# Performance work log

Measured on AMD Instinct MI355X. Metric: run time of the kernel, lower is better.

Reference implementation:

```python
import jax, jax.numpy as jnp
import numpy as np

B, N, H = 32, 2048, 128


def _lstm_step(c, h, x, Wi, Wh, b):
    # flax LSTMCell: gates i,f,g,o; sigmoid/sigmoid/tanh/sigmoid
    gates = x @ Wi + h @ Wh + b  # (B,N,4H)
    i, f, g, o = jnp.split(gates, 4, axis=-1)
    c_new = jax.nn.sigmoid(f) * c + jax.nn.sigmoid(i) * jnp.tanh(g)
    h_new = jax.nn.sigmoid(o) * jnp.tanh(c_new)
    return c_new, h_new


def setup_inputs() -> dict:
    key = jax.random.key(0)
    ks = jax.random.split(key, 24)
    f32 = jnp.float32
    inp = {}
    inp['node_embeddings'] = jax.random.normal(ks[0], (B, N, H), f32)
    for nm, k in zip(['hs_c0', 'hs_h0', 'hs_c1', 'hs_h1'], ks[1:5]):
        inp[nm] = jax.random.normal(k, (B, N, H), f32)
    ip = jax.random.uniform(ks[5], (B, N), f32)
    inp['instruction_pointer'] = ip / jnp.sum(ip, axis=-1, keepdims=True)
    inp['Wi0'] = jax.random.normal(ks[6], (H, 4 * H), f32) * 0.05
    inp['Wh0'] = jax.random.normal(ks[7], (H, 4 * H), f32) * 0.05
    inp['b0'] = jnp.zeros((4 * H,), f32)
    inp['Wi1'] = jax.random.normal(ks[8], (H, 4 * H), f32) * 0.05
    inp['Wh1'] = jax.random.normal(ks[9], (H, 4 * H), f32) * 0.05
    inp['b1'] = jnp.zeros((4 * H,), f32)
    inp['W_raise'] = jax.random.normal(ks[10], (4 * H, 2), f32) * 0.05
    inp['b_raise'] = jnp.zeros((2,), f32)
    inp['W_branch'] = jax.random.normal(ks[11], (4 * H, 2), f32) * 0.05
    inp['b_branch'] = jnp.zeros((2,), f32)
    inp['true_indexes'] = jax.random.randint(ks[12], (B, N), 0, N, jnp.int32)
    inp['false_indexes'] = jax.random.randint(ks[13], (B, N), 0, N, jnp.int32)
    inp['raise_indexes'] = jax.random.randint(ks[14], (B, N), 0, N, jnp.int32)
    inp['exit_node_indexes'] = jax.random.randint(ks[15], (B,), 0, N, jnp.int32)
    inp['raise_node_indexes'] = jax.random.randint(ks[16], (B,), 0, N, jnp.int32)
    inp['step_limits'] = jax.random.randint(ks[17], (B,), 0, 100, jnp.int32)
    inp['current_step'] = 5
    return inp


def reference(node_embeddings, hs_c0, hs_h0, hs_c1, hs_h1, instruction_pointer,
              Wi0, Wh0, b0, Wi1, Wh1, b1, W_raise, b_raise, W_branch, b_branch,
              true_indexes, false_indexes, raise_indexes,
              exit_node_indexes, raise_node_indexes, step_limits, current_step):
    bidx = jnp.arange(B)
    old = [hs_c0, hs_h0, hs_c1, hs_h1]

    # execute: per-node 2-layer stacked LSTM (vectorized over B,N)
    c0n, h0n = _lstm_step(hs_c0, hs_h0, node_embeddings, Wi0, Wh0, b0)
    c1n, h1n = _lstm_step(hs_c1, hs_h1, h0n, Wi1, Wh1, b1)
    contrib = [c0n, h0n, c1n, h1n]

    # mask_h: keep old state at exit node and (raise_in_ipagnn) at raise node
    def mask_nodes(hc, ho, idx):
        return hc.at[bidx, idx].set(ho[bidx, idx])
    contrib = [mask_nodes(mask_nodes(hc, ho, exit_node_indexes), ho, raise_node_indexes)
               for hc, ho in zip(contrib, old)]

    hs_emb = jnp.concatenate(contrib, axis=-1)  # (B,N,4H)

    raise_dec = jax.nn.softmax(hs_emb @ W_raise + b_raise, axis=-1)
    zero_one = jnp.array([0.0, 1.0], dtype=raise_dec.dtype)
    raise_dec = raise_dec.at[bidx, exit_node_indexes].set(zero_one)
    raise_dec = raise_dec.at[bidx, raise_node_indexes].set(zero_one)
    branch_dec = jax.nn.softmax(hs_emb @ W_branch + b_branch, axis=-1)

    p_raise = raise_dec[..., 0]
    p_noraise = raise_dec[..., 1]
    p_true = p_noraise * branch_dec[..., 0]
    p_false = p_noraise * branch_dec[..., 1]

    seg = jax.vmap(lambda v, idx: jax.ops.segment_sum(v, idx, num_segments=N))
    ip = instruction_pointer
    ip_new = (seg(p_raise * ip, raise_indexes)
              + seg(p_true * ip, true_indexes)
              + seg(p_false * ip, false_indexes))  # (B,N)
    denom = (ip_new + 1e-7)[..., None]

    wr = (p_raise * ip)[..., None]
    wt = (p_true * ip)[..., None]
    wf = (p_false * ip)[..., None]

    def agg(h):
        return (seg(h * wr, raise_indexes) + seg(h * wt, true_indexes)
                + seg(h * wf, false_indexes)) / denom
    hs_new = [agg(h) for h in contrib]

    # keep_old_if_done
    not_done = (current_step < step_limits)  # (B,)
    hs_out = [jnp.where(not_done[:, None, None], hn, ho) for hn, ho in zip(hs_new, old)]
    ip_out = jnp.where(not_done[:, None], ip_new, ip)

    # pack carry: (c0,h0,c1,h1, instruction_pointer) -> (B,N,4H+1)
    return jnp.concatenate(hs_out + [ip_out[..., None]], axis=-1)
```

## Files before the change

kernel.cpp:

```cpp
#include <hip/hip_runtime.h>
#include <stdint.h>

#define BB 32
#define NN 2048
#define HH 128
#define BN (BB*NN)

typedef short v8s __attribute__((ext_vector_type(8)));
typedef float v4f __attribute__((ext_vector_type(4)));

__device__ __forceinline__ unsigned short f2b(float f){
  union { float f; unsigned int i; } v; v.f = f;
  unsigned int x = v.i;
  unsigned int r = x + 0x7FFFu + ((x >> 16) & 1u);
  return (unsigned short)(r >> 16);
}
__device__ __forceinline__ unsigned int pk2(float a, float b){
  return (unsigned int)f2b(a) | ((unsigned int)f2b(b) << 16);
}
__device__ __forceinline__ float sigm(float x){ return 1.0f / (1.0f + __expf(-x)); }

__global__ void kswz(const float* __restrict__ Wi0, const float* __restrict__ Wh0,
                     const float* __restrict__ Wi1, const float* __restrict__ Wh1,
                     unsigned short* __restrict__ Bsw0, unsigned short* __restrict__ Bsw1){
  int bid = blockIdx.x;
  int layer = bid >> 8;
  int kc = (bid >> 5) & 7;
  int ct = bid & 31;
  int lane = threadIdx.x;
  const float* Wi = layer ? Wi1 : Wi0;
  const float* Wh = layer ? Wh1 : Wh0;
  unsigned short* dst = layer ? Bsw1 : Bsw0;
  int col = ct*16 + (lane & 15);
  int kbase = kc*32 + (lane >> 4)*8;
  size_t o = ((size_t)(kc*32 + ct)*64 + (size_t)lane)*8;
  #pragma unroll
  for (int j = 0; j < 8; j++){
    int k = kbase + j;
    dst[o + j] = f2b((k < 128) ? Wi[k*512 + col] : Wh[(k-128)*512 + col]);
  }
}

__global__ void ksave(const float* __restrict__ c0, const float* __restrict__ h0,
                      const float* __restrict__ c1, const float* __restrict__ h1,
                      const int* __restrict__ exit_idx, const int* __restrict__ raise_idx,
                      float* __restrict__ saved){
  int b = blockIdx.x, which = blockIdx.y, c = threadIdx.x;
  int idx = which ? raise_idx[b] : exit_idx[b];
  size_t row = (size_t)b*NN + idx;
  const float* bufs[4] = {c0, h0, c1, h1};
  saved[((size_t)b*2 + which)*512 + c] = bufs[c >> 7][row*128 + (c & 127)];
}

__global__ void krestore(float* c0, float* h0, float* c1, float* h1,
                         const int* __restrict__ exit_idx, const int* __restrict__ raise_idx,
                         const float* __restrict__ saved){
  int b = blockIdx.x, which = blockIdx.y, c = threadIdx.x;
  int idx = which ? raise_idx[b] : exit_idx[b];
  size_t row = (size_t)b*NN + idx;
  float* bufs[4] = {c0, h0, c1, h1};
  bufs[c >> 7][row*128 + (c & 127)] = saved[((size_t)b*2 + which)*512 + c];
}

#define ROWSB 64
#define PA 264
#define PH 136

__global__ __launch_bounds__(512, 4) void klstm2(
    const float* __restrict__ ne,
    float* __restrict__ c0, float* __restrict__ h0,
    float* __restrict__ c1, float* __restrict__ h1,
    const unsigned short* __restrict__ Bsw0, const float* __restrict__ b0,
    const unsigned short* __restrict__ Bsw1, const float* __restrict__ b1,
    const int* __restrict__ step_limits, const int* __restrict__ cur_step)
{
  __shared__ unsigned short ldsA[ROWSB*PA];
  __shared__ unsigned short ldsH[ROWSB*PH];

  int rowbase = blockIdx.x * ROWSB;
  int b = rowbase >> 11;
  if (cur_step[0] >= step_limits[b]) return;

  int tid = threadIdx.x;
  int wid = tid >> 6, lane = tid & 63;
  int quad = lane >> 4, l16 = lane & 15;

  {
    int srow = tid >> 6;
    int scol = (tid & 63) * 4;
    #pragma unroll
    for (int p = 0; p < 8; p++){
      int row = p*8 + srow;
      size_t g = (size_t)(rowbase + row)*128 + (scol & 127);
      const float* src = (scol < 128) ? (ne + g) : (h0 + g);
      float4 v = *(const float4*)src;
      uint2 w; w.x = pk2(v.x, v.y); w.y = pk2(v.z, v.w);
      *(uint2*)&ldsA[row*PA + scol] = w;
    }
    int hrow = tid >> 5;
    int hcol = (tid & 31) * 4;
    #pragma unroll
    for (int p = 0; p < 4; p++){
      int row = p*16 + hrow;
      float4 v = *(const float4*)(h1 + (size_t)(rowbase + row)*128 + hcol);
      uint2 w; w.x = pk2(v.x, v.y); w.y = pk2(v.z, v.w);
      *(uint2*)&ldsH[row*PH + hcol] = w;
    }
  }
  __syncthreads();

  int ch = wid*16 + l16;

  v4f acc[4][4] = {};
  #pragma unroll
  for (int kc = 0; kc < 8; kc++){
    v8s bf0 = ((const v8s*)Bsw0)[(size_t)(kc*32 + 0*8 + wid)*64 + lane];
    v8s bf1 = ((const v8s*)Bsw0)[(size_t)(kc*32 + 1*8 + wid)*64 + lane];
    v8s bf2 = ((const v8s*)Bsw0)[(size_t)(kc*32 + 2*8 + wid)*64 + lane];
    v8s bf3 = ((const v8s*)Bsw0)[(size_t)(kc*32 + 3*8 + wid)*64 + lane];
    #pragma unroll
    for (int rt = 0; rt < 4; rt++){
      v8s a = *(const v8s*)&ldsA[(rt*16 + l16)*PA + kc*32 + quad*8];
      acc[rt][0] = __builtin_amdgcn_mfma_f32_16x16x32_bf16(a, bf0, acc[rt][0], 0,0,0);
      acc[rt][1] = __builtin_amdgcn_mfma_f32_16x16x32_bf16(a, bf1, acc[rt][1], 0,0,0);
      acc[rt][2] = __builtin_amdgcn_mfma_f32_16x16x32_bf16(a, bf2, acc[rt][2], 0,0,0);
      acc[rt][3] = __builtin_amdgcn_mfma_f32_16x16x32_bf16(a, bf3, acc[rt][3], 0,0,0);
    }
  }
  __syncthreads();

  {
    float bi = b0[ch], bfv = b0[128+ch], bg = b0[256+ch], bo = b0[384+ch];
    #pragma unroll
    for (int rt = 0; rt < 4; rt++){
      #pragma unroll
      for (int r = 0; r < 4; r++){
        int lrow = rt*16 + quad*4 + r;
        size_t row = (size_t)rowbase + lrow;
        float iv = acc[rt][0][r] + bi;
        float fv = acc[rt][1][r] + bfv;
        float gv = acc[rt][2][r] + bg;
        float ov = acc[rt][3][r] + bo;
        float cold = c0[row*128 + ch];
        float cn = sigm(fv)*cold + sigm(iv)*tanhf(gv);
        float hn = sigm(ov)*tanhf(cn);
        c0[row*128 + ch] = cn;
        h0[row*128 + ch] = hn;
        ldsA[lrow*PA + ch] = f2b(hn);
      }
    }
  }
  __syncthreads();

  #pragma unroll
  for (int rt = 0; rt < 4; rt++)
    #pragma unroll
    for (int g = 0; g < 4; g++)
      acc[rt][g] = (v4f){0.f, 0.f, 0.f, 0.f};

  #pragma unroll
  for (int kc = 0; kc < 8; kc++){
    v8s bf0 = ((const v8s*)Bsw1)[(size_t)(kc*32 + 0*8 + wid)*64 + lane];
    v8s bf1 = ((const v8s*)Bsw1)[(size_t)(kc*32 + 1*8 + wid)*64 + lane];
    v8s bf2 = ((const v8s*)Bsw1)[(size_t)(kc*32 + 2*8 + wid)*64 + lane];
    v8s bf3 = ((const v8s*)Bsw1)[(size_t)(kc*32 + 3*8 + wid)*64 + lane];
    #pragma unroll
    for (int rt = 0; rt < 4; rt++){
      v8s a = (kc < 4)
        ? *(const v8s*)&ldsA[(rt*16 + l16)*PA + kc*32 + quad*8]
        : *(const v8s*)&ldsH[(rt*16 + l16)*PH + (kc-4)*32 + quad*8];
      acc[rt][0] = __builtin_amdgcn_mfma_f32_16x16x32_bf16(a, bf0, acc[rt][0], 0,0,0);
      acc[rt][1] = __builtin_amdgcn_mfma_f32_16x16x32_bf16(a, bf1, acc[rt][1], 0,0,0);
      acc[rt][2] = __builtin_amdgcn_mfma_f32_16x16x32_bf16(a, bf2, acc[rt][2], 0,0,0);
      acc[rt][3] = __builtin_amdgcn_mfma_f32_16x16x32_bf16(a, bf3, acc[rt][3], 0,0,0);
    }
  }

  {
    float bi = b1[ch], bfv = b1[128+ch], bg = b1[256+ch], bo = b1[384+ch];
    #pragma unroll
    for (int rt = 0; rt < 4; rt++){
      #pragma unroll
      for (int r = 0; r < 4; r++){
        size_t row = (size_t)rowbase + rt*16 + quad*4 + r;
        float iv = acc[rt][0][r] + bi;
        float fv = acc[rt][1][r] + bfv;
        float gv = acc[rt][2][r] + bg;
        float ov = acc[rt][3][r] + bo;
        float cold = c1[row*128 + ch];
        float cn = sigm(fv)*cold + sigm(iv)*tanhf(gv);
        float hn = sigm(ov)*tanhf(cn);
        c1[row*128 + ch] = cn;
        h1[row*128 + ch] = hn;
      }
    }
  }
}

__global__ __launch_bounds__(256) void kdec(
    const float* __restrict__ c0, const float* __restrict__ h0,
    const float* __restrict__ c1, const float* __restrict__ h1,
    const float* __restrict__ Wr, const float* __restrict__ br,
    const float* __restrict__ Wb, const float* __restrict__ bb,
    const float* __restrict__ ip,
    const int* __restrict__ exit_idx, const int* __restrict__ raise_idx,
    float* __restrict__ wbuf)
{
  int tid = threadIdx.x;
  int wid = tid >> 6, lane = tid & 63;
  int gid = blockIdx.x*4 + wid;
  int b = gid >> 11, n = gid & 2047;

  const float* bufs[4] = {c0, h0, c1, h1};
  const float* hb = bufs[lane >> 4] + (size_t)gid*128 + (lane & 15)*8;
  float4 hv0 = *(const float4*)hb;
  float4 hv1 = *(const float4*)(hb + 4);
  float hv[8] = {hv0.x, hv0.y, hv0.z, hv0.w, hv1.x, hv1.y, hv1.z, hv1.w};
  const float* wrp = Wr + lane*16;
  const float* wbp = Wb + lane*16;
  float r0=0.f, r1=0.f, q0=0.f, q1=0.f;
  #pragma unroll
  for (int j = 0; j < 8; j++){
    float h = hv[j];
    r0 += h * wrp[j*2];  r1 += h * wrp[j*2+1];
    q0 += h * wbp[j*2];  q1 += h * wbp[j*2+1];
  }
  #pragma unroll
  for (int off = 32; off > 0; off >>= 1){
    r0 += __shfl_xor(r0, off, 64);
    r1 += __shfl_xor(r1, off, 64);
    q0 += __shfl_xor(q0, off, 64);
    q1 += __shfl_xor(q1, off, 64);
  }
  if (lane == 0){
    r0 += br[0]; r1 += br[1];
    q0 += bb[0]; q1 += bb[1];
    float pr, pn;
    if (n == exit_idx[b] || n == raise_idx[b]){ pr = 0.f; pn = 1.f; }
    else {
      float m = fmaxf(r0, r1);
      float e0 = __expf(r0 - m), e1 = __expf(r1 - m);
      pr = e0 / (e0 + e1); pn = e1 / (e0 + e1);
    }
    float m2 = fmaxf(q0, q1);
    float f0 = __expf(q0 - m2), f1 = __expf(q1 - m2);
    float pt = f0 / (f0 + f1), pf = f1 / (f0 + f1);
    float ipv = ip[gid];
    wbuf[0*BN + gid] = pr * ipv;
    wbuf[1*BN + gid] = pn * pt * ipv;
    wbuf[2*BN + gid] = pn * pf * ipv;
  }
}

__global__ void kcount(const int* __restrict__ ri, const int* __restrict__ ti,
                       const int* __restrict__ fi, int* __restrict__ counts){
  int gid = blockIdx.x*256 + threadIdx.x;
  int base = (gid >> 11) << 11;
  atomicAdd(&counts[base + ri[gid]], 1);
  atomicAdd(&counts[base + ti[gid]], 1);
  atomicAdd(&counts[base + fi[gid]], 1);
}

__global__ __launch_bounds__(256) void kscan(const int* __restrict__ counts,
                                             int* __restrict__ offsets){
  __shared__ int lds[256];
  int b = blockIdx.x, tid = threadIdx.x;
  const int* c = counts + b*NN;
  int* o = offsets + b*NN;
  int v[8]; int s = 0;
  #pragma unroll
  for (int i = 0; i < 8; i++){ v[i] = c[tid*8+i]; s += v[i]; }
  lds[tid] = s;
  __syncthreads();
  if (tid == 0){
    int run = 0;
    for (int t = 0; t < 256; t++){ int tmp = lds[t]; lds[t] = run; run += tmp; }
  }
  __syncthreads();
  int off = lds[tid];
  #pragma unroll
  for (int i = 0; i < 8; i++){ o[tid*8+i] = off; off += v[i]; }
}

__global__ void kfill(const int* __restrict__ ri, const int* __restrict__ ti,
                      const int* __restrict__ fi, const int* __restrict__ offsets,
                      int* __restrict__ cursor, unsigned short* __restrict__ edges){
  int gid = blockIdx.x*256 + threadIdx.x;
  int b = gid >> 11, n = gid & 2047;
  size_t ebase = (size_t)b*3*NN;
  int t0 = ri[gid]; int p0 = atomicAdd(&cursor[b*NN+t0], 1);
  edges[ebase + offsets[b*NN+t0] + p0] = (unsigned short)(n);
  int t1 = ti[gid]; int p1 = atomicAdd(&cursor[b*NN+t1], 1);
  edges[ebase + offsets[b*NN+t1] + p1] = (unsigned short)(n | (1<<11));
  int t2 = fi[gid]; int p2 = atomicAdd(&cursor[b*NN+t2], 1);
  edges[ebase + offsets[b*NN+t2] + p2] = (unsigned short)(n | (2<<11));
}

__global__ __launch_bounds__(128) void kagg(
    const float* __restrict__ c0, const float* __restrict__ h0,
    const float* __restrict__ c1, const float* __restrict__ h1,
    const float* __restrict__ ip,
    const float* __restrict__ wbuf, const unsigned short* __restrict__ edges,
    const int* __restrict__ counts, const int* __restrict__ offsets,
    const int* __restrict__ step_limits, const int* __restrict__ cur_step,
    float* __restrict__ out)
{
  int gid = blockIdx.x;
  int b = gid >> 11;
  int tid = threadIdx.x;
  size_t obase = (size_t)gid*513;
  const float* bufs[4] = {c0, h0, c1, h1};

  if (cur_step[0] >= step_limits[b]){
    int c = tid*4;
    const float* s = bufs[c >> 7];
    size_t rb = (size_t)gid*128 + (c & 127);
    out[obase + c+0] = s[rb+0];
    out[obase + c+1] = s[rb+1];
    out[obase + c+2] = s[rb+2];
    out[obase + c+3] = s[rb+3];
    if (tid == 0) out[obase + 512] = ip[gid];
    return;
  }

  int cnt = counts[gid], off = offsets[gid];
  const unsigned short* eb = edges + (size_t)b*3*NN + off;
  const float* sb = bufs[tid >> 5];
  int coff = (tid & 31)*4;
  float a0=0.f, a1=0.f, a2=0.f, a3=0.f, ipn=0.f;
  for (int e = 0; e < cnt; e++){
    int pk = eb[e];
    int n = pk & 2047, et = pk >> 11;
    float w = wbuf[et*BN + (b<<11) + n];
    ipn += w;
    float4 sv = *(const float4*)(sb + ((size_t)(b<<11) + n)*128 + coff);
    a0 += w * sv.x;
    a1 += w * sv.y;
    a2 += w * sv.z;
    a3 += w * sv.w;
  }
  int c = tid*4;
  float inv = 1.0f / (ipn + 1e-7f);
  out[obase + c+0] = a0*inv;
  out[obase + c+1] = a1*inv;
  out[obase + c+2] = a2*inv;
  out[obase + c+3] = a3*inv;
  if (tid == 0) out[obase + 512] = ipn;
}

extern "C" void kernel_launch(void* const* d_in, const int* in_sizes, int n_in,
                              void* d_out, int out_size, void* d_ws, size_t ws_size,
                              hipStream_t stream){
  const float* ne  = (const float*)d_in[0];
  float* c0  = (float*)d_in[1];
  float* h0  = (float*)d_in[2];
  float* c1  = (float*)d_in[3];
  float* h1  = (float*)d_in[4];
  const float* ip  = (const float*)d_in[5];
  const float* Wi0 = (const float*)d_in[6];
  const float* Wh0 = (const float*)d_in[7];
  const float* b0  = (const float*)d_in[8];
  const float* Wi1 = (const float*)d_in[9];
  const float* Wh1 = (const float*)d_in[10];
  const float* b1  = (const float*)d_in[11];
  const float* Wr  = (const float*)d_in[12];
  const float* br  = (const float*)d_in[13];
  const float* Wb  = (const float*)d_in[14];
  const float* bb  = (const float*)d_in[15];
  const int* ti  = (const int*)d_in[16];
  const int* fi  = (const int*)d_in[17];
  const int* ri  = (const int*)d_in[18];
  const int* ei  = (const int*)d_in[19];
  const int* rni = (const int*)d_in[20];
  const int* sl  = (const int*)d_in[21];
  const int* cs  = (const int*)d_in[22];
  float* out = (float*)d_out;

  uint8_t* ws = (uint8_t*)d_ws;
  unsigned short* Bsw0    = (unsigned short*)(ws + 0);
  unsigned short* Bsw1    = (unsigned short*)(ws + 262144);
  float*          saved   = (float*)(ws + 524288);
  float*          wbuf    = (float*)(ws + 655360);
  int*            counts  = (int*)(ws + 1441792);
  int*            offsets = (int*)(ws + 1703936);
  int*            cursor  = (int*)(ws + 1966080);
  unsigned short* edges   = (unsigned short*)(ws + 2228224);

  hipMemsetAsync(counts, 0, BN*sizeof(int), stream);
  hipMemsetAsync(cursor, 0, BN*sizeof(int), stream);

  kswz<<<512, 64, 0, stream>>>(Wi0, Wh0, Wi1, Wh1, Bsw0, Bsw1);
  ksave<<<dim3(BB, 2), 512, 0, stream>>>(c0, h0, c1, h1, ei, rni, saved);

  klstm2<<<BN/ROWSB, 512, 0, stream>>>(ne, c0, h0, c1, h1, Bsw0, b0, Bsw1, b1, sl, cs);

  krestore<<<dim3(BB, 2), 512, 0, stream>>>(c0, h0, c1, h1, ei, rni, saved);

  kdec<<<BN/4, 256, 0, stream>>>(c0, h0, c1, h1, Wr, br, Wb, bb, ip, ei, rni, wbuf);

  kcount<<<BN/256, 256, 0, stream>>>(ri, ti, fi, counts);
  kscan<<<BB, 256, 0, stream>>>(counts, offsets);
  kfill<<<BN/256, 256, 0, stream>>>(ri, ti, fi, offsets, cursor, edges);

  kagg<<<BN, 128, 0, stream>>>(c0, h0, c1, h1, ip, wbuf, edges, counts, offsets,
                               sl, cs, out);
}
```

Measured before the change: 496.8 us.

## Halve LSTM tile rows, prefetch weight fragments, fast activations, fuse edge counting into decoder

The LSTM kernel now processes 32 rows per block instead of 64. This doubles the grid and cuts accumulator registers. It prefetches the next K-chunk of B fragments and preloads the cell state and bias before the matmul. Layer-0 h goes to a separate LDS buffer, which removes one barrier. Sigmoid and tanh now use the hardware reciprocal plus exp approximations, at some cost in accuracy. The separate edge-count kernel is folded into the decoder kernel using idle lanes, which saves one launch.

```diff
diff --git a/kernel.cpp b/kernel.cpp
--- a/kernel.cpp
+++ b/kernel.cpp
@@ -18,7 +18,9 @@
 __device__ __forceinline__ unsigned int pk2(float a, float b){
   return (unsigned int)f2b(a) | ((unsigned int)f2b(b) << 16);
 }
-__device__ __forceinline__ float sigm(float x){ return 1.0f / (1.0f + __expf(-x)); }
+__device__ __forceinline__ float frcp(float x){ return __builtin_amdgcn_rcpf(x); }
+__device__ __forceinline__ float fsigm(float x){ return frcp(1.0f + __expf(-x)); }
+__device__ __forceinline__ float ftanh(float x){ return 1.0f - 2.0f*frcp(1.0f + __expf(2.0f*x)); }
 
 __global__ void kswz(const float* __restrict__ Wi0, const float* __restrict__ Wh0,
                      const float* __restrict__ Wi1, const float* __restrict__ Wh1,
@@ -62,7 +64,7 @@
   bufs[c >> 7][row*128 + (c & 127)] = saved[((size_t)b*2 + which)*512 + c];
 }
 
-#define ROWSB 64
+#define ROWSB 32
 #define PA 264
 #define PH 136
 
@@ -76,6 +78,7 @@
 {
   __shared__ unsigned short ldsA[ROWSB*PA];
   __shared__ unsigned short ldsH[ROWSB*PH];
+  __shared__ unsigned short ldsG[ROWSB*PH];
 
   int rowbase = blockIdx.x * ROWSB;
   int b = rowbase >> 11;
@@ -84,115 +87,132 @@
   int tid = threadIdx.x;
   int wid = tid >> 6, lane = tid & 63;
   int quad = lane >> 4, l16 = lane & 15;
-
-  {
-    int srow = tid >> 6;
-    int scol = (tid & 63) * 4;
-    #pragma unroll
-    for (int p = 0; p < 8; p++){
-      int row = p*8 + srow;
-      size_t g = (size_t)(rowbase + row)*128 + (scol & 127);
-      const float* src = (scol < 128) ? (ne + g) : (h0 + g);
-      float4 v = *(const float4*)src;
-      uint2 w; w.x = pk2(v.x, v.y); w.y = pk2(v.z, v.w);
-      *(uint2*)&ldsA[row*PA + scol] = w;
-    }
-    int hrow = tid >> 5;
-    int hcol = (tid & 31) * 4;
-    #pragma unroll
-    for (int p = 0; p < 4; p++){
-      int row = p*16 + hrow;
-      float4 v = *(const float4*)(h1 + (size_t)(rowbase + row)*128 + hcol);
-      uint2 w; w.x = pk2(v.x, v.y); w.y = pk2(v.z, v.w);
-      *(uint2*)&ldsH[row*PH + hcol] = w;
-    }
+  int ch = wid*16 + l16;
+
+  #pragma unroll
+  for (int p = 0; p < 4; p++){
+    int idx = p*512 + tid;
+    int row = idx >> 6, chunk = idx & 63;
+    size_t g = (size_t)(rowbase + row)*128 + (chunk & 31)*4;
+    float4 v = (chunk < 32) ? *(const float4*)(ne + g) : *(const float4*)(h0 + g);
+    uint2 w; w.x = pk2(v.x, v.y); w.y = pk2(v.z, v.w);
+    *(uint2*)&ldsA[row*PA + chunk*4] = w;
   }
   __syncthreads();
 
-  int ch = wid*16 + l16;
-
-  v4f acc[4][4] = {};
+  float cpre[8], bias[4];
+  #pragma unroll
+  for (int rt = 0; rt < 2; rt++)
+    #pragma unroll
+    for (int r = 0; r < 4; r++)
+      cpre[rt*4+r] = c0[((size_t)rowbase + rt*16 + quad*4 + r)*128 + ch];
+  #pragma unroll
+  for (int g = 0; g < 4; g++) bias[g] = b0[g*128 + ch];
+
+  #pragma unroll
+  for (int p = 0; p < 2; p++){
+    int idx = p*512 + tid;
+    int row = idx >> 5, chunk = idx & 31;
+    float4 v = *(const float4*)(h1 + (size_t)(rowbase + row)*128 + chunk*4);
+    uint2 w; w.x = pk2(v.x, v.y); w.y = pk2(v.z, v.w);
+    *(uint2*)&ldsH[row*PH + chunk*4] = w;
+  }
+
+  const v8s* Bv0 = (const v8s*)Bsw0;
+  v4f acc[2][4] = {};
+  v8s bc[4], bn[4];
+  #pragma unroll
+  for (int g = 0; g < 4; g++) bc[g] = Bv0[(size_t)(g*8 + wid)*64 + lane];
   #pragma unroll
   for (int kc = 0; kc < 8; kc++){
-    v8s bf0 = ((const v8s*)Bsw0)[(size_t)(kc*32 + 0*8 + wid)*64 + lane];
-    v8s bf1 = ((const v8s*)Bsw0)[(size_t)(kc*32 + 1*8 + wid)*64 + lane];
-    v8s bf2 = ((const v8s*)Bsw0)[(size_t)(kc*32 + 2*8 + wid)*64 + lane];
-    v8s bf3 = ((const v8s*)Bsw0)[(size_t)(kc*32 + 3*8 + wid)*64 + lane];
-    #pragma unroll
-    for (int rt = 0; rt < 4; rt++){
-      v8s a = *(const v8s*)&ldsA[(rt*16 + l16)*PA + kc*32 + quad*8];
-      acc[rt][0] = __builtin_amdgcn_mfma_f32_16x16x32_bf16(a, bf0, acc[rt][0], 0,0,0);
-      acc[rt][1] = __builtin_amdgcn_mfma_f32_16x16x32_bf16(a, bf1, acc[rt][1], 0,0,0);
-      acc[rt][2] = __builtin_amdgcn_mfma_f32_16x16x32_bf16(a, bf2, acc[rt][2], 0,0,0);
-      acc[rt][3] = __builtin_amdgcn_mfma_f32_16x16x32_bf16(a, bf3, acc[rt][3], 0,0,0);
+    if (kc < 7){
+      #pragma unroll
+      for (int g = 0; g < 4; g++) bn[g] = Bv0[(size_t)((kc+1)*32 + g*8 + wid)*64 + lane];
+    }
+    v8s a0 = *(const v8s*)&ldsA[(0*16 + l16)*PA + kc*32 + quad*8];
+    v8s a1 = *(const v8s*)&ldsA[(1*16 + l16)*PA + kc*32 + quad*8];
+    #pragma unroll
+    for (int g = 0; g < 4; g++){
+      acc[0][g] = __builtin_amdgcn_mfma_f32_16x16x32_bf16(a0, bc[g], acc[0][g], 0,0,0);
+      acc[1][g] = __builtin_amdgcn_mfma_f32_16x16x32_bf16(a1, bc[g], acc[1][g], 0,0,0);
+    }
+    #pragma unroll
+    for (int g = 0; g < 4; g++) bc[g] = bn[g];
+  }
+
+  #pragma unroll
+  for (int rt = 0; rt < 2; rt++){
+    #pragma unroll
+    for (int r = 0; r < 4; r++){
+      int lrow = rt*16 + quad*4 + r;
+      size_t row = (size_t)rowbase + lrow;
+      float iv = acc[rt][0][r] + bias[0];
+      float fv = acc[rt][1][r] + bias[1];
+      float gv = acc[rt][2][r] + bias[2];
+      float ov = acc[rt][3][r] + bias[3];
+      float cold = cpre[rt*4+r];
+      float cn = fsigm(fv)*cold + fsigm(iv)*ftanh(gv);
+      float hn = fsigm(ov)*ftanh(cn);
+      c0[row*128 + ch] = cn;
+      h0[row*128 + ch] = hn;
+      ldsG[lrow*PH + ch] = f2b(hn);
     }
   }
   __syncthreads();
 
-  {
-    float bi = b0[ch], bfv = b0[128+ch], bg = b0[256+ch], bo = b0[384+ch];
-    #pragma unroll
-    for (int rt = 0; rt < 4; rt++){
-      #pragma unroll
-      for (int r = 0; r < 4; r++){
-        int lrow = rt*16 + quad*4 + r;
-        size_t row = (size_t)rowbase + lrow;
-        float iv = acc[rt][0][r] + bi;
-        float fv = acc[rt][1][r] + bfv;
-        float gv = acc[rt][2][r] + bg;
-        float ov = acc[rt][3][r] + bo;
-        float cold = c0[row*128 + ch];
-        float cn = sigm(fv)*cold + sigm(iv)*tanhf(gv);
-        float hn = sigm(ov)*tanhf(cn);
-        c0[row*128 + ch] = cn;
-        h0[row*128 + ch] = hn;
-        ldsA[lrow*PA + ch] = f2b(hn);
-      }
-    }
-  }
-  __syncthreads();
-
-  #pragma unroll
-  for (int rt = 0; rt < 4; rt++)
+  #pragma unroll
+  for (int rt = 0; rt < 2; rt++)
+    #pragma unroll
+    for (int r = 0; r < 4; r++)
+      cpre[rt*4+r] = c1[((size_t)rowbase + rt*16 + quad*4 + r)*128 + ch];
+  #pragma unroll
+  for (int g = 0; g < 4; g++) bias[g] = b1[g*128 + ch];
+
+  const v8s* Bv1 = (const v8s*)Bsw1;
+  #pragma unroll
+  for (int rt = 0; rt < 2; rt++)
     #pragma unroll
     for (int g = 0; g < 4; g++)
       acc[rt][g] = (v4f){0.f, 0.f, 0.f, 0.f};
-
+  #pragma unroll
+  for (int g = 0; g < 4; g++) bc[g] = Bv1[(size_t)(g*8 + wid)*64 + lane];
   #pragma unroll
   for (int kc = 0; kc < 8; kc++){
-    v8s bf0 = ((const v8s*)Bsw1)[(size_t)(kc*32 + 0*8 + wid)*64 + lane];
-    v8s bf1 = ((const v8s*)Bsw1)[(size_t)(kc*32 + 1*8 + wid)*64 + lane];
-    v8s bf2 = ((const v8s*)Bsw1)[(size_t)(kc*32 + 2*8 + wid)*64 + lane];
-    v8s bf3 = ((const v8s*)Bsw1)[(size_t)(kc*32 + 3*8 + wid)*64 + lane];
-    #pragma unroll
-    for (int rt = 0; rt < 4; rt++){
-      v8s a = (kc < 4)
-        ? *(const v8s*)&ldsA[(rt*16 + l16)*PA + kc*32 + quad*8]
-        : *(const v8s*)&ldsH[(rt*16 + l16)*PH + (kc-4)*32 + quad*8];
-      acc[rt][0] = __builtin_amdgcn_mfma_f32_16x16x32_bf16(a, bf0, acc[rt][0], 0,0,0);
-      acc[rt][1] = __builtin_amdgcn_mfma_f32_16x16x32_bf16(a, bf1, acc[rt][1], 0,0,0);
-      acc[rt][2] = __builtin_amdgcn_mfma_f32_16x16x32_bf16(a, bf2, acc[rt][2], 0,0,0);
-      acc[rt][3] = __builtin_amdgcn_mfma_f32_16x16x32_bf16(a, bf3, acc[rt][3], 0,0,0);
-    }
-  }
-
-  {
-    float bi = b1[ch], bfv = b1[128+ch], bg = b1[256+ch], bo = b1[384+ch];
-    #pragma unroll
-    for (int rt = 0; rt < 4; rt++){
+    if (kc < 7){
       #pragma unroll
-      for (int r = 0; r < 4; r++){
-        size_t row = (size_t)rowbase + rt*16 + quad*4 + r;
-        float iv = acc[rt][0][r] + bi;
-        float fv = acc[rt][1][r] + bfv;
-        float gv = acc[rt][2][r] + bg;
-        float ov = acc[rt][3][r] + bo;
-        float cold = c1[row*128 + ch];
-        float cn = sigm(fv)*cold + sigm(iv)*tanhf(gv);
-        float hn = sigm(ov)*tanhf(cn);
-        c1[row*128 + ch] = cn;
-        h1[row*128 + ch] = hn;
-      }
+      for (int g = 0; g < 4; g++) bn[g] = Bv1[(size_t)((kc+1)*32 + g*8 + wid)*64 + lane];
+    }
+    v8s a0, a1;
+    if (kc < 4){
+      a0 = *(const v8s*)&ldsG[(0*16 + l16)*PH + kc*32 + quad*8];
+      a1 = *(const v8s*)&ldsG[(1*16 + l16)*PH + kc*32 + quad*8];
+    } else {
+      a0 = *(const v8s*)&ldsH[(0*16 + l16)*PH + (kc-4)*32 + quad*8];
+      a1 = *(const v8s*)&ldsH[(1*16 + l16)*PH + (kc-4)*32 + quad*8];
+    }
+    #pragma unroll
+    for (int g = 0; g < 4; g++){
+      acc[0][g] = __builtin_amdgcn_mfma_f32_16x16x32_bf16(a0, bc[g], acc[0][g], 0,0,0);
+      acc[1][g] = __builtin_amdgcn_mfma_f32_16x16x32_bf16(a1, bc[g], acc[1][g], 0,0,0);
+    }
+    #pragma unroll
+    for (int g = 0; g < 4; g++) bc[g] = bn[g];
+  }
+
+  #pragma unroll
+  for (int rt = 0; rt < 2; rt++){
+    #pragma unroll
+    for (int r = 0; r < 4; r++){
+      size_t row = (size_t)rowbase + rt*16 + quad*4 + r;
+      float iv = acc[rt][0][r] + bias[0];
+      float fv = acc[rt][1][r] + bias[1];
+      float gv = acc[rt][2][r] + bias[2];
+      float ov = acc[rt][3][r] + bias[3];
+      float cold = cpre[rt*4+r];
+      float cn = fsigm(fv)*cold + fsigm(iv)*ftanh(gv);
+      float hn = fsigm(ov)*ftanh(cn);
+      c1[row*128 + ch] = cn;
+      h1[row*128 + ch] = hn;
     }
   }
 }
@@ -204,6 +224,8 @@
     const float* __restrict__ Wb, const float* __restrict__ bb,
     const float* __restrict__ ip,
     const int* __restrict__ exit_idx, const int* __restrict__ raise_idx,
+    const int* __restrict__ ri, const int* __restrict__ ti, const int* __restrict__ fi,
+    int* __restrict__ counts,
     float* __restrict__ wbuf)
 {
   int tid = threadIdx.x;
@@ -249,16 +271,13 @@
     wbuf[0*BN + gid] = pr * ipv;
     wbuf[1*BN + gid] = pn * pt * ipv;
     wbuf[2*BN + gid] = pn * pf * ipv;
-  }
-}
-
-__global__ void kcount(const int* __restrict__ ri, const int* __restrict__ ti,
-                       const int* __restrict__ fi, int* __restrict__ counts){
-  int gid = blockIdx.x*256 + threadIdx.x;
-  int base = (gid >> 11) << 11;
-  atomicAdd(&counts[base + ri[gid]], 1);
-  atomicAdd(&counts[base + ti[gid]], 1);
-  atomicAdd(&counts[base + fi[gid]], 1);
+  } else if (lane == 1){
+    atomicAdd(&counts[(b<<11) + ri[gid]], 1);
+  } else if (lane == 2){
+    atomicAdd(&counts[(b<<11) + ti[gid]], 1);
+  } else if (lane == 3){
+    atomicAdd(&counts[(b<<11) + fi[gid]], 1);
+  }
 }
 
 __global__ __launch_bounds__(256) void kscan(const int* __restrict__ counts,
@@ -396,9 +415,9 @@
 
   krestore<<<dim3(BB, 2), 512, 0, stream>>>(c0, h0, c1, h1, ei, rni, saved);
 
-  kdec<<<BN/4, 256, 0, stream>>>(c0, h0, c1, h1, Wr, br, Wb, bb, ip, ei, rni, wbuf);
-
-  kcount<<<BN/256, 256, 0, stream>>>(ri, ti, fi, counts);
+  kdec<<<BN/4, 256, 0, stream>>>(c0, h0, c1, h1, Wr, br, Wb, bb, ip, ei, rni,
+                                 ri, ti, fi, counts, wbuf);
+
   kscan<<<BB, 256, 0, stream>>>(counts, offsets);
   kfill<<<BN/256, 256, 0, stream>>>(ri, ti, fi, offsets, cursor, edges);
 
```

Result: faster. 463.5 us (-6.7%).
